# Optimization experiments

Hardware: AMD Instinct MI355X
Metric: run time of the kernel (lower is better)

## Reference

```python
import jax, jax.numpy as jnp
import numpy as np

N_NODES = 100000
N_EDGES = 1600000
ATOM_DIM = 16
POS_DIM = 3
HID = 128


def _linear_init(key, fan_in, fan_out):
    # torch nn.Linear default: U(-1/sqrt(fan_in), 1/sqrt(fan_in)) for W and b
    kw, kb = jax.random.split(key)
    bound = 1.0 / np.sqrt(fan_in)
    W = jax.random.uniform(kw, (fan_in, fan_out), jnp.float32, -bound, bound)
    b = jax.random.uniform(kb, (fan_out,), jnp.float32, -bound, bound)
    return W, b


def setup_inputs() -> dict:
    key = jax.random.key(0)
    ks = jax.random.split(key, 8)
    x = jax.random.normal(ks[0], (N_NODES, ATOM_DIM), jnp.float32)
    pos = jax.random.normal(ks[1], (N_NODES, POS_DIM), jnp.float32)
    edge_index = jax.random.randint(ks[2], (2, N_EDGES), 0, N_NODES, jnp.int64 if jax.config.jax_enable_x64 else jnp.int32)
    Wa, ba = _linear_init(ks[3], ATOM_DIM, HID)
    Wp, bp = _linear_init(ks[4], POS_DIM, HID)
    W1, b1 = _linear_init(ks[5], 2 * HID + 1, HID)
    W2, b2 = _linear_init(ks[6], HID, HID)
    W3, b3 = _linear_init(ks[7], HID, 4)
    return {"x": x, "pos": pos, "edge_index": edge_index,
            "Wa": Wa, "ba": ba, "Wp": Wp, "bp": bp,
            "W1": W1, "b1": b1, "W2": W2, "b2": b2, "W3": W3, "b3": b3}


def reference(x, pos, edge_index, Wa, ba, Wp, bp, W1, b1, W2, b2, W3, b3):
    # node embeddings: atom_emb + pos_emb, [N, HID]
    node_emb = (x @ Wa + ba) + (pos @ Wp + bp)
    src, dst = edge_index[0], edge_index[1]
    source_emb = node_emb[src]            # [E, HID]
    target_emb = node_emb[dst]            # [E, HID]
    diff = pos[src] - pos[dst]            # [E, 3]
    distances = jnp.linalg.norm(diff, axis=-1, keepdims=True)  # [E, 1]
    edge_input = jnp.concatenate([source_emb, target_emb, distances], axis=-1)  # [E, 2*HID+1]
    h = jax.nn.silu(edge_input @ W1 + b1)
    h = jax.nn.silu(h @ W2 + b2)
    bond_logits = h @ W3 + b3             # [E, 4]
    return bond_logits
```

## Files before the change

### kernel.cpp

```cpp
#include <hip/hip_runtime.h>
#include <hip/hip_bf16.h>
#include <hip/hip_fp16.h>

typedef _Float16 half8 __attribute__((ext_vector_type(8)));
typedef __fp16 fp16x2 __attribute__((ext_vector_type(2)));
typedef float floatx4 __attribute__((ext_vector_type(4)));

#define HID 128
#define TILE_M 64
#define LDH 136

__device__ __forceinline__ float fast_silu(float v) {
    float e = __expf(-v);
    return v * __builtin_amdgcn_rcpf(1.f + e);
}

__device__ __forceinline__ unsigned int pk2(float a, float b) {
    fp16x2 h = __builtin_amdgcn_cvt_pkrtz(a, b);
    return __builtin_bit_cast(unsigned int, h);
}

__global__ __launch_bounds__(256) void node_emb_kernel(
    const float* __restrict__ x, const float* __restrict__ pos,
    const float* __restrict__ Wa, const float* __restrict__ ba,
    const float* __restrict__ Wp, const float* __restrict__ bp,
    _Float16* __restrict__ nodeEmb, int N)
{
    __shared__ float sWa[16 * HID];
    __shared__ float sWp[3 * HID];
    __shared__ float sb[HID];
    for (int i = threadIdx.x; i < 16 * HID; i += 256) sWa[i] = Wa[i];
    for (int i = threadIdx.x; i < 3 * HID;  i += 256) sWp[i] = Wp[i];
    for (int i = threadIdx.x; i < HID;      i += 256) sb[i] = ba[i] + bp[i];
    __syncthreads();

    int total = N * 16;
    for (int gid = blockIdx.x * 256 + threadIdx.x; gid < total;
         gid += gridDim.x * 256) {
        int n  = gid >> 4;
        int c0 = (gid & 15) * 8;
        const float* xr = x + (size_t)n * 16;
        const float* pr = pos + (size_t)n * 3;
        float xv[16];
        #pragma unroll
        for (int k = 0; k < 4; ++k) {
            float4 v = *(const float4*)(xr + k * 4);
            xv[k*4] = v.x; xv[k*4+1] = v.y; xv[k*4+2] = v.z; xv[k*4+3] = v.w;
        }
        float p0 = pr[0], p1 = pr[1], p2 = pr[2];
        half8 o;
        #pragma unroll
        for (int i = 0; i < 8; ++i) {
            int c = c0 + i;
            float s = sb[c];
            #pragma unroll
            for (int k = 0; k < 16; ++k) s += xv[k] * sWa[k * HID + c];
            s += p0 * sWp[c] + p1 * sWp[HID + c] + p2 * sWp[2 * HID + c];
            o[i] = (_Float16)s;
        }
        *(half8*)(nodeEmb + (size_t)n * HID + c0) = o;
    }
}

__global__ __launch_bounds__(256, 2) void edge_mlp_kernel(
    const _Float16* __restrict__ nodeEmb,
    const float* __restrict__ pos,
    const int* __restrict__ eidx,
    const float* __restrict__ W1, const float* __restrict__ b1,
    const float* __restrict__ W2, const float* __restrict__ b2,
    const float* __restrict__ W3, const float* __restrict__ b3,
    float* __restrict__ out, int E, int nTiles)
{
    __shared__ __align__(16) _Float16 sA[2 * TILE_M * HID];
    __shared__ __align__(16) _Float16 sH1[TILE_M][LDH];
    __shared__ __align__(16) _Float16 sH2[TILE_M][LDH];
    __shared__ float sDist[TILE_M];

    const int t    = threadIdx.x;
    const int wave = t >> 6;
    const int lane = t & 63;
    const int quad = lane >> 4;
    const int l16  = lane & 15;
    const int colbase = wave * 32;

    half8 w1f[8][2];
    half8 w2f[4][2];
    half8 w3f[4];
    float w1c[2][4], b1f[2][4], b2f[2][4];
    #pragma unroll
    for (int ct = 0; ct < 2; ++ct) {
        int col = colbase + ct * 16 + l16;
        #pragma unroll
        for (int kc = 0; kc < 8; ++kc)
            #pragma unroll
            for (int j = 0; j < 8; ++j)
                w1f[kc][ct][j] = (_Float16)W1[(kc * 32 + quad * 8 + j) * HID + col];
        #pragma unroll
        for (int kc = 0; kc < 4; ++kc)
            #pragma unroll
            for (int j = 0; j < 8; ++j)
                w2f[kc][ct][j] = (_Float16)W2[(kc * 32 + quad * 8 + j) * HID + col];
        #pragma unroll
        for (int i = 0; i < 4; ++i) {
            int c2 = colbase + ct * 16 + quad * 4 + i;
            w1c[ct][i] = W1[256 * HID + c2];
            b1f[ct][i] = b1[c2];
            b2f[ct][i] = b2[c2];
        }
    }
    #pragma unroll
    for (int kc = 0; kc < 4; ++kc)
        #pragma unroll
        for (int j = 0; j < 8; ++j)
            w3f[kc][j] = (_Float16)W3[(kc * 32 + quad * 8 + j) * 4 + (l16 & 3)];
    const float b3v0 = b3[0], b3v1 = b3[1], b3v2 = b3[2], b3v3 = b3[3];

    int nid[8];
    float dpre = 0.f;

    auto load_nid = [&](int tl) {
        int eb = tl * TILE_M;
        #pragma unroll
        for (int i = 0; i < 8; ++i) {
            int cid = i * 256 + t;
            int row = cid >> 4;
            int r   = row & 63;
            int e   = eb + r; if (e >= E) e = E - 1;
            nid[i] = (row >> 6) ? eidx[(size_t)E + e] : eidx[e];
        }
    };
    auto load_dist = [&](int tl) -> float {
        if (t >= TILE_M) return 0.f;
        int e = tl * TILE_M + t; if (e >= E) e = E - 1;
        int s = eidx[e], d = eidx[(size_t)E + e];
        float dx = pos[3 * (size_t)s]     - pos[3 * (size_t)d];
        float dy = pos[3 * (size_t)s + 1] - pos[3 * (size_t)d + 1];
        float dz = pos[3 * (size_t)s + 2] - pos[3 * (size_t)d + 2];
        return sqrtf(dx * dx + dy * dy + dz * dz);
    };
    auto dma_issue = [&]() {
        #pragma unroll
        for (int i = 0; i < 8; ++i) {
            int cid = i * 256 + t;
            int row = cid >> 4;
            int cg  = (cid & 15) ^ (row & 15);
            const _Float16* gp = nodeEmb + (size_t)nid[i] * HID + cg * 8;
            __builtin_amdgcn_global_load_lds(
                (__attribute__((address_space(1))) void*)gp,
                (__attribute__((address_space(3))) void*)&sA[(i * 256 + (t & 192)) * 8],
                16, 0, 0);
        }
    };

    bool havePrev = false;
    int prevEbase = 0;
    int tile = blockIdx.x;
    if (tile < nTiles) {
        load_nid(tile);
        dpre = load_dist(tile);
        dma_issue();
    }

    for (; tile < nTiles; tile += gridDim.x) {
        const int ebase = tile * TILE_M;
        if (t < TILE_M) sDist[t] = dpre;
        __syncthreads();

        if (havePrev) {
            floatx4 acc3 = (floatx4){0.f, 0.f, 0.f, 0.f};
            #pragma unroll
            for (int kc = 0; kc < 4; ++kc) {
                half8 h = *(const half8*)&sH2[wave * 16 + l16][kc * 32 + quad * 8];
                acc3 = __builtin_amdgcn_mfma_f32_16x16x32_f16(w3f[kc], h, acc3, 0, 0, 0);
            }
            if (quad == 0) {
                int e = prevEbase + wave * 16 + l16;
                if (e < E) {
                    float4 o = {acc3[0] + b3v0, acc3[1] + b3v1,
                                acc3[2] + b3v2, acc3[3] + b3v3};
                    *(float4*)&out[(size_t)e * 4] = o;
                }
            }
        }

        int nxt = tile + gridDim.x;
        if (nxt < nTiles) {
            load_nid(nxt);
            dpre = load_dist(nxt);
        }

        floatx4 acc[2][4];
        #pragma unroll
        for (int ct = 0; ct < 2; ++ct)
            #pragma unroll
            for (int rt = 0; rt < 4; ++rt) {
                acc[ct][rt][0] = b1f[ct][0]; acc[ct][rt][1] = b1f[ct][1];
                acc[ct][rt][2] = b1f[ct][2]; acc[ct][rt][3] = b1f[ct][3];
            }
        #pragma unroll
        for (int kc = 0; kc < 8; ++kc) {
            int hf   = kc >> 2;
            int cg   = (kc & 3) * 4 + quad;
            int slot = (cg ^ l16) * 8;
            const _Float16* base = &sA[(hf * TILE_M + l16) * HID + slot];
            half8 a0 = *(const half8*)(base + 0 * 16 * HID);
            half8 a1 = *(const half8*)(base + 1 * 16 * HID);
            half8 a2 = *(const half8*)(base + 2 * 16 * HID);
            half8 a3 = *(const half8*)(base + 3 * 16 * HID);
            acc[0][0] = __builtin_amdgcn_mfma_f32_16x16x32_f16(w1f[kc][0], a0, acc[0][0], 0, 0, 0);
            acc[0][1] = __builtin_amdgcn_mfma_f32_16x16x32_f16(w1f[kc][0], a1, acc[0][1], 0, 0, 0);
            acc[0][2] = __builtin_amdgcn_mfma_f32_16x16x32_f16(w1f[kc][0], a2, acc[0][2], 0, 0, 0);
            acc[0][3] = __builtin_amdgcn_mfma_f32_16x16x32_f16(w1f[kc][0], a3, acc[0][3], 0, 0, 0);
            acc[1][0] = __builtin_amdgcn_mfma_f32_16x16x32_f16(w1f[kc][1], a0, acc[1][0], 0, 0, 0);
            acc[1][1] = __builtin_amdgcn_mfma_f32_16x16x32_f16(w1f[kc][1], a1, acc[1][1], 0, 0, 0);
            acc[1][2] = __builtin_amdgcn_mfma_f32_16x16x32_f16(w1f[kc][1], a2, acc[1][2], 0, 0, 0);
            acc[1][3] = __builtin_amdgcn_mfma_f32_16x16x32_f16(w1f[kc][1], a3, acc[1][3], 0, 0, 0);
        }
        #pragma unroll
        for (int rt = 0; rt < 4; ++rt) {
            int m = rt * 16 + l16;
            float d = sDist[m];
            #pragma unroll
            for (int ct = 0; ct < 2; ++ct) {
                float v0 = fast_silu(fmaf(d, w1c[ct][0], acc[ct][rt][0]));
                float v1 = fast_silu(fmaf(d, w1c[ct][1], acc[ct][rt][1]));
                float v2 = fast_silu(fmaf(d, w1c[ct][2], acc[ct][rt][2]));
                float v3 = fast_silu(fmaf(d, w1c[ct][3], acc[ct][rt][3]));
                uint2 w;
                w.x = pk2(v0, v1);
                w.y = pk2(v2, v3);
                *(uint2*)&sH1[m][colbase + ct * 16 + quad * 4] = w;
            }
        }
        __syncthreads();

        if (nxt < nTiles) dma_issue();

        floatx4 acc2[2][4];
        #pragma unroll
        for (int ct = 0; ct < 2; ++ct)
            #pragma unroll
            for (int rt = 0; rt < 4; ++rt) {
                acc2[ct][rt][0] = b2f[ct][0]; acc2[ct][rt][1] = b2f[ct][1];
                acc2[ct][rt][2] = b2f[ct][2]; acc2[ct][rt][3] = b2f[ct][3];
            }
        #pragma unroll
        for (int kc = 0; kc < 4; ++kc) {
            int kin = kc * 32 + quad * 8;
            half8 a0 = *(const half8*)&sH1[l16][kin];
            half8 a1 = *(const half8*)&sH1[16 + l16][kin];
            half8 a2 = *(const half8*)&sH1[32 + l16][kin];
            half8 a3 = *(const half8*)&sH1[48 + l16][kin];
            acc2[0][0] = __builtin_amdgcn_mfma_f32_16x16x32_f16(w2f[kc][0], a0, acc2[0][0], 0, 0, 0);
            acc2[0][1] = __builtin_amdgcn_mfma_f32_16x16x32_f16(w2f[kc][0], a1, acc2[0][1], 0, 0, 0);
            acc2[0][2] = __builtin_amdgcn_mfma_f32_16x16x32_f16(w2f[kc][0], a2, acc2[0][2], 0, 0, 0);
            acc2[0][3] = __builtin_amdgcn_mfma_f32_16x16x32_f16(w2f[kc][0], a3, acc2[0][3], 0, 0, 0);
            acc2[1][0] = __builtin_amdgcn_mfma_f32_16x16x32_f16(w2f[kc][1], a0, acc2[1][0], 0, 0, 0);
            acc2[1][1] = __builtin_amdgcn_mfma_f32_16x16x32_f16(w2f[kc][1], a1, acc2[1][1], 0, 0, 0);
            acc2[1][2] = __builtin_amdgcn_mfma_f32_16x16x32_f16(w2f[kc][1], a2, acc2[1][2], 0, 0, 0);
            acc2[1][3] = __builtin_amdgcn_mfma_f32_16x16x32_f16(w2f[kc][1], a3, acc2[1][3], 0, 0, 0);
        }
        #pragma unroll
        for (int rt = 0; rt < 4; ++rt) {
            int m = rt * 16 + l16;
            #pragma unroll
            for (int ct = 0; ct < 2; ++ct) {
                float v0 = fast_silu(acc2[ct][rt][0]);
                float v1 = fast_silu(acc2[ct][rt][1]);
                float v2 = fast_silu(acc2[ct][rt][2]);
                float v3 = fast_silu(acc2[ct][rt][3]);
                uint2 w;
                w.x = pk2(v0, v1);
                w.y = pk2(v2, v3);
                *(uint2*)&sH2[m][colbase + ct * 16 + quad * 4] = w;
            }
        }
        havePrev = true;
        prevEbase = ebase;
    }

    if (havePrev) {
        __syncthreads();
        floatx4 acc3 = (floatx4){0.f, 0.f, 0.f, 0.f};
        #pragma unroll
        for (int kc = 0; kc < 4; ++kc) {
            half8 h = *(const half8*)&sH2[wave * 16 + l16][kc * 32 + quad * 8];
            acc3 = __builtin_amdgcn_mfma_f32_16x16x32_f16(w3f[kc], h, acc3, 0, 0, 0);
        }
        if (quad == 0) {
            int e = prevEbase + wave * 16 + l16;
            if (e < E) {
                float4 o = {acc3[0] + b3v0, acc3[1] + b3v1,
                            acc3[2] + b3v2, acc3[3] + b3v3};
                *(float4*)&out[(size_t)e * 4] = o;
            }
        }
    }
}

extern "C" void kernel_launch(void* const* d_in, const int* in_sizes, int n_in,
                              void* d_out, int out_size, void* d_ws, size_t ws_size,
                              hipStream_t stream) {
    const float* x   = (const float*)d_in[0];
    const float* pos = (const float*)d_in[1];
    const int*  eidx = (const int*)d_in[2];
    const float* Wa = (const float*)d_in[3];
    const float* ba = (const float*)d_in[4];
    const float* Wp = (const float*)d_in[5];
    const float* bp = (const float*)d_in[6];
    const float* W1 = (const float*)d_in[7];
    const float* b1 = (const float*)d_in[8];
    const float* W2 = (const float*)d_in[9];
    const float* b2 = (const float*)d_in[10];
    const float* W3 = (const float*)d_in[11];
    const float* b3 = (const float*)d_in[12];
    float* out = (float*)d_out;

    int N = in_sizes[0] / 16;
    int E = in_sizes[2] / 2;

    _Float16* nodeEmb = (_Float16*)d_ws;

    int nodeBlocks = (N * 16 + 255) / 256;
    node_emb_kernel<<<nodeBlocks, 256, 0, stream>>>(x, pos, Wa, ba, Wp, bp, nodeEmb, N);

    int nTiles = (E + TILE_M - 1) / TILE_M;
    edge_mlp_kernel<<<512, 256, 0, stream>>>(nodeEmb, pos, eidx,
                                             W1, b1, W2, b2, W3, b3,
                                             out, E, nTiles);
}
```

Measured before the change: 348.9 us.

## Use MFMA for node embedding, fuse final layer via dot2, swizzle LDS, raise occupancy

The node-embedding kernel now runs as one MFMA per 16x16 tile, with the 19 input features zero-padded to K=32, replacing the scalar FMA loop over shared-memory weights. In the edge kernel, the last 128->4 layer is folded into the layer-2 epilogue using packed fp16 dot2 and cross-lane shuffles. Per-wave partial sums go to a small LDS buffer, so the sH2 tile and its MFMA pass are gone. sH1 drops padding for an XOR-swizzled layout, and the saved LDS lets occupancy rise to 3 blocks per SIMD with 768 blocks. This risks register pressure at the higher occupancy and changes rounding, since x and pos are now converted to fp16 before the embedding.

Result: slower. 762.5 us (+118.6%).

```diff
diff --git a/kernel.cpp b/kernel.cpp
--- a/kernel.cpp
+++ b/kernel.cpp
@@ -3,12 +3,12 @@
 #include <hip/hip_fp16.h>
 
 typedef _Float16 half8 __attribute__((ext_vector_type(8)));
+typedef _Float16 half4 __attribute__((ext_vector_type(4)));
 typedef __fp16 fp16x2 __attribute__((ext_vector_type(2)));
 typedef float floatx4 __attribute__((ext_vector_type(4)));
 
 #define HID 128
 #define TILE_M 64
-#define LDH 136
 
 __device__ __forceinline__ float fast_silu(float v) {
     float e = __expf(-v);
@@ -18,6 +18,14 @@
 __device__ __forceinline__ unsigned int pk2(float a, float b) {
     fp16x2 h = __builtin_amdgcn_cvt_pkrtz(a, b);
     return __builtin_bit_cast(unsigned int, h);
+}
+
+__device__ __forceinline__ float dot2f(fp16x2 a, fp16x2 b, float c) {
+#if __has_builtin(__builtin_amdgcn_fdot2)
+    return __builtin_amdgcn_fdot2(a, b, c, false);
+#else
+    return fmaf((float)a[0], (float)b[0], fmaf((float)a[1], (float)b[1], c));
+#endif
 }
 
 __global__ __launch_bounds__(256) void node_emb_kernel(
@@ -26,43 +34,72 @@
     const float* __restrict__ Wp, const float* __restrict__ bp,
     _Float16* __restrict__ nodeEmb, int N)
 {
-    __shared__ float sWa[16 * HID];
-    __shared__ float sWp[3 * HID];
-    __shared__ float sb[HID];
-    for (int i = threadIdx.x; i < 16 * HID; i += 256) sWa[i] = Wa[i];
-    for (int i = threadIdx.x; i < 3 * HID;  i += 256) sWp[i] = Wp[i];
-    for (int i = threadIdx.x; i < HID;      i += 256) sb[i] = ba[i] + bp[i];
-    __syncthreads();
-
-    int total = N * 16;
-    for (int gid = blockIdx.x * 256 + threadIdx.x; gid < total;
-         gid += gridDim.x * 256) {
-        int n  = gid >> 4;
-        int c0 = (gid & 15) * 8;
-        const float* xr = x + (size_t)n * 16;
-        const float* pr = pos + (size_t)n * 3;
-        float xv[16];
-        #pragma unroll
-        for (int k = 0; k < 4; ++k) {
-            float4 v = *(const float4*)(xr + k * 4);
-            xv[k*4] = v.x; xv[k*4+1] = v.y; xv[k*4+2] = v.z; xv[k*4+3] = v.w;
-        }
-        float p0 = pr[0], p1 = pr[1], p2 = pr[2];
-        half8 o;
-        #pragma unroll
-        for (int i = 0; i < 8; ++i) {
-            int c = c0 + i;
-            float s = sb[c];
-            #pragma unroll
-            for (int k = 0; k < 16; ++k) s += xv[k] * sWa[k * HID + c];
-            s += p0 * sWp[c] + p1 * sWp[HID + c] + p2 * sWp[2 * HID + c];
-            o[i] = (_Float16)s;
-        }
-        *(half8*)(nodeEmb + (size_t)n * HID + c0) = o;
-    }
-}
-
-__global__ __launch_bounds__(256, 2) void edge_mlp_kernel(
+    const int wave = threadIdx.x >> 6;
+    const int lane = threadIdx.x & 63;
+    const int quad = lane >> 4;
+    const int l16  = lane & 15;
+
+    half8 wf[8];
+    floatx4 bias[8];
+    #pragma unroll
+    for (int ct = 0; ct < 8; ++ct) {
+        int col = ct * 16 + l16;
+        #pragma unroll
+        for (int j = 0; j < 8; ++j) {
+            int k = quad * 8 + j;
+            float w = 0.f;
+            if (k < 16) w = Wa[k * HID + col];
+            else if (k < 19) w = Wp[(k - 16) * HID + col];
+            wf[ct][j] = (_Float16)w;
+        }
+        #pragma unroll
+        for (int i = 0; i < 4; ++i) {
+            int c2 = ct * 16 + quad * 4 + i;
+            bias[ct][i] = ba[c2] + bp[c2];
+        }
+    }
+
+    int nTiles = (N + 63) >> 6;
+    for (int tile = blockIdx.x * 4 + wave; tile < nTiles; tile += gridDim.x * 4) {
+        half8 af[4];
+        #pragma unroll
+        for (int rt = 0; rt < 4; ++rt) {
+            int node = tile * 64 + rt * 16 + l16;
+            int nd = node < N ? node : N - 1;
+            half8 a = (half8){0, 0, 0, 0, 0, 0, 0, 0};
+            if (quad < 2) {
+                const float* xp = x + (size_t)nd * 16 + quad * 8;
+                float4 v0 = *(const float4*)xp;
+                float4 v1 = *(const float4*)(xp + 4);
+                a[0] = (_Float16)v0.x; a[1] = (_Float16)v0.y;
+                a[2] = (_Float16)v0.z; a[3] = (_Float16)v0.w;
+                a[4] = (_Float16)v1.x; a[5] = (_Float16)v1.y;
+                a[6] = (_Float16)v1.z; a[7] = (_Float16)v1.w;
+            } else if (quad == 2) {
+                const float* pp = pos + (size_t)nd * 3;
+                a[0] = (_Float16)pp[0]; a[1] = (_Float16)pp[1]; a[2] = (_Float16)pp[2];
+            }
+            af[rt] = a;
+        }
+        #pragma unroll
+        for (int ct = 0; ct < 8; ++ct) {
+            #pragma unroll
+            for (int rt = 0; rt < 4; ++rt) {
+                int node = tile * 64 + rt * 16 + l16;
+                floatx4 d = bias[ct];
+                d = __builtin_amdgcn_mfma_f32_16x16x32_f16(wf[ct], af[rt], d, 0, 0, 0);
+                if (node < N) {
+                    half4 hv;
+                    hv[0] = (_Float16)d[0]; hv[1] = (_Float16)d[1];
+                    hv[2] = (_Float16)d[2]; hv[3] = (_Float16)d[3];
+                    *(half4*)(nodeEmb + (size_t)node * HID + ct * 16 + quad * 4) = hv;
+                }
+            }
+        }
+    }
+}
+
+__global__ __launch_bounds__(256, 3) void edge_mlp_kernel(
     const _Float16* __restrict__ nodeEmb,
     const float* __restrict__ pos,
     const int* __restrict__ eidx,
@@ -72,8 +109,8 @@
     float* __restrict__ out, int E, int nTiles)
 {
     __shared__ __align__(16) _Float16 sA[2 * TILE_M * HID];
-    __shared__ __align__(16) _Float16 sH1[TILE_M][LDH];
-    __shared__ __align__(16) _Float16 sH2[TILE_M][LDH];
+    __shared__ __align__(16) _Float16 sH1[TILE_M * HID];
+    __shared__ float pf[4][TILE_M][4];
     __shared__ float sDist[TILE_M];
 
     const int t    = threadIdx.x;
@@ -85,7 +122,7 @@
 
     half8 w1f[8][2];
     half8 w2f[4][2];
-    half8 w3f[4];
+    fp16x2 w3h[2][2][4];
     float w1c[2][4], b1f[2][4], b2f[2][4];
     #pragma unroll
     for (int ct = 0; ct < 2; ++ct) {
@@ -107,13 +144,19 @@
             b1f[ct][i] = b1[c2];
             b2f[ct][i] = b2[c2];
         }
-    }
-    #pragma unroll
-    for (int kc = 0; kc < 4; ++kc)
-        #pragma unroll
-        for (int j = 0; j < 8; ++j)
-            w3f[kc][j] = (_Float16)W3[(kc * 32 + quad * 8 + j) * 4 + (l16 & 3)];
-    const float b3v0 = b3[0], b3v1 = b3[1], b3v2 = b3[2], b3v3 = b3[3];
+        #pragma unroll
+        for (int pr = 0; pr < 2; ++pr) {
+            int c0 = colbase + ct * 16 + quad * 4 + pr * 2;
+            #pragma unroll
+            for (int n = 0; n < 4; ++n) {
+                fp16x2 h;
+                h[0] = (__fp16)W3[c0 * 4 + n];
+                h[1] = (__fp16)W3[(c0 + 1) * 4 + n];
+                w3h[ct][pr][n] = h;
+            }
+        }
+    }
+    const float b3n = b3[t & 3];
 
     int nid[8];
     float dpre = 0.f;
@@ -167,20 +210,10 @@
         __syncthreads();
 
         if (havePrev) {
-            floatx4 acc3 = (floatx4){0.f, 0.f, 0.f, 0.f};
-            #pragma unroll
-            for (int kc = 0; kc < 4; ++kc) {
-                half8 h = *(const half8*)&sH2[wave * 16 + l16][kc * 32 + quad * 8];
-                acc3 = __builtin_amdgcn_mfma_f32_16x16x32_f16(w3f[kc], h, acc3, 0, 0, 0);
-            }
-            if (quad == 0) {
-                int e = prevEbase + wave * 16 + l16;
-                if (e < E) {
-                    float4 o = {acc3[0] + b3v0, acc3[1] + b3v1,
-                                acc3[2] + b3v2, acc3[3] + b3v3};
-                    *(float4*)&out[(size_t)e * 4] = o;
-                }
-            }
+            int m = t >> 2, n = t & 3;
+            float s = pf[0][m][n] + pf[1][m][n] + pf[2][m][n] + pf[3][m][n] + b3n;
+            int e = prevEbase + m;
+            if (e < E) out[(size_t)e * 4 + n] = s;
         }
 
         int nxt = tile + gridDim.x;
@@ -229,7 +262,9 @@
                 uint2 w;
                 w.x = pk2(v0, v1);
                 w.y = pk2(v2, v3);
-                *(uint2*)&sH1[m][colbase + ct * 16 + quad * 4] = w;
+                int cgb  = wave * 4 + ct * 2 + (quad >> 1);
+                int slot = cgb ^ l16;
+                *(uint2*)&sH1[m * HID + slot * 8 + (quad & 1) * 4] = w;
             }
         }
         __syncthreads();
@@ -246,11 +281,11 @@
             }
         #pragma unroll
         for (int kc = 0; kc < 4; ++kc) {
-            int kin = kc * 32 + quad * 8;
-            half8 a0 = *(const half8*)&sH1[l16][kin];
-            half8 a1 = *(const half8*)&sH1[16 + l16][kin];
-            half8 a2 = *(const half8*)&sH1[32 + l16][kin];
-            half8 a3 = *(const half8*)&sH1[48 + l16][kin];
+            int slot = ((kc * 4 + quad) ^ l16) * 8;
+            half8 a0 = *(const half8*)&sH1[(0 * 16 + l16) * HID + slot];
+            half8 a1 = *(const half8*)&sH1[(1 * 16 + l16) * HID + slot];
+            half8 a2 = *(const half8*)&sH1[(2 * 16 + l16) * HID + slot];
+            half8 a3 = *(const half8*)&sH1[(3 * 16 + l16) * HID + slot];
             acc2[0][0] = __builtin_amdgcn_mfma_f32_16x16x32_f16(w2f[kc][0], a0, acc2[0][0], 0, 0, 0);
             acc2[0][1] = __builtin_amdgcn_mfma_f32_16x16x32_f16(w2f[kc][0], a1, acc2[0][1], 0, 0, 0);
             acc2[0][2] = __builtin_amdgcn_mfma_f32_16x16x32_f16(w2f[kc][0], a2, acc2[0][2], 0, 0, 0);
@@ -260,19 +295,31 @@
             acc2[1][2] = __builtin_amdgcn_mfma_f32_16x16x32_f16(w2f[kc][1], a2, acc2[1][2], 0, 0, 0);
             acc2[1][3] = __builtin_amdgcn_mfma_f32_16x16x32_f16(w2f[kc][1], a3, acc2[1][3], 0, 0, 0);
         }
+
         #pragma unroll
         for (int rt = 0; rt < 4; ++rt) {
             int m = rt * 16 + l16;
+            float p0 = 0.f, p1 = 0.f, p2 = 0.f, p3 = 0.f;
             #pragma unroll
             for (int ct = 0; ct < 2; ++ct) {
                 float v0 = fast_silu(acc2[ct][rt][0]);
                 float v1 = fast_silu(acc2[ct][rt][1]);
                 float v2 = fast_silu(acc2[ct][rt][2]);
                 float v3 = fast_silu(acc2[ct][rt][3]);
-                uint2 w;
-                w.x = pk2(v0, v1);
-                w.y = pk2(v2, v3);
-                *(uint2*)&sH2[m][colbase + ct * 16 + quad * 4] = w;
+                fp16x2 hA = __builtin_amdgcn_cvt_pkrtz(v0, v1);
+                fp16x2 hB = __builtin_amdgcn_cvt_pkrtz(v2, v3);
+                p0 = dot2f(hA, w3h[ct][0][0], p0); p0 = dot2f(hB, w3h[ct][1][0], p0);
+                p1 = dot2f(hA, w3h[ct][0][1], p1); p1 = dot2f(hB, w3h[ct][1][1], p1);
+                p2 = dot2f(hA, w3h[ct][0][2], p2); p2 = dot2f(hB, w3h[ct][1][2], p2);
+                p3 = dot2f(hA, w3h[ct][0][3], p3); p3 = dot2f(hB, w3h[ct][1][3], p3);
+            }
+            p0 += __shfl_xor(p0, 16); p0 += __shfl_xor(p0, 32);
+            p1 += __shfl_xor(p1, 16); p1 += __shfl_xor(p1, 32);
+            p2 += __shfl_xor(p2, 16); p2 += __shfl_xor(p2, 32);
+            p3 += __shfl_xor(p3, 16); p3 += __shfl_xor(p3, 32);
+            if (quad == 0) {
+                float4 o = {p0, p1, p2, p3};
+                *(float4*)&pf[wave][m][0] = o;
             }
         }
         havePrev = true;
@@ -281,20 +328,10 @@
 
     if (havePrev) {
         __syncthreads();
-        floatx4 acc3 = (floatx4){0.f, 0.f, 0.f, 0.f};
-        #pragma unroll
-        for (int kc = 0; kc < 4; ++kc) {
-            half8 h = *(const half8*)&sH2[wave * 16 + l16][kc * 32 + quad * 8];
-            acc3 = __builtin_amdgcn_mfma_f32_16x16x32_f16(w3f[kc], h, acc3, 0, 0, 0);
-        }
-        if (quad == 0) {
-            int e = prevEbase + wave * 16 + l16;
-            if (e < E) {
-                float4 o = {acc3[0] + b3v0, acc3[1] + b3v1,
-                            acc3[2] + b3v2, acc3[3] + b3v3};
-                *(float4*)&out[(size_t)e * 4] = o;
-            }
-        }
+        int m = t >> 2, n = t & 3;
+        float s = pf[0][m][n] + pf[1][m][n] + pf[2][m][n] + pf[3][m][n] + b3n;
+        int e = prevEbase + m;
+        if (e < E) out[(size_t)e * 4 + n] = s;
     }
 }
 
@@ -321,11 +358,12 @@
 
     _Float16* nodeEmb = (_Float16*)d_ws;
 
-    int nodeBlocks = (N * 16 + 255) / 256;
+    int nodeTiles = (N + 63) / 64;
+    int nodeBlocks = (nodeTiles + 3) / 4;
     node_emb_kernel<<<nodeBlocks, 256, 0, stream>>>(x, pos, Wa, ba, Wp, bp, nodeEmb, N);
 
     int nTiles = (E + TILE_M - 1) / TILE_M;
-    edge_mlp_kernel<<<512, 256, 0, stream>>>(nodeEmb, pos, eidx,
+    edge_mlp_kernel<<<768, 256, 0, stream>>>(nodeEmb, pos, eidx,
                                              W1, b1, W2, b2, W3, b3,
                                              out, E, nTiles);
 }
```
